# Kernel tuning notes

Hardware: AMD Instinct MI355X
Metric: run time of the kernel (lower is better)

## Reference

```python
import jax, jax.numpy as jnp
import numpy as np


def setup_inputs() -> dict:
    key = jax.random.key(0)
    k1, k2 = jax.random.split(key)
    N, H, W, F = 32, 16, 16, 256
    B, C = 64, 8
    x = jax.random.normal(k1, (N, H, W, F), dtype=jnp.float32)
    # keras 'uniform' initializer: U(-0.05, 0.05)
    T = jax.random.uniform(k2, (F, B, C), dtype=jnp.float32, minval=-0.05, maxval=0.05)
    return {"x": x, "T": T}


def reference(x, T):
    # x: [N,H,W,F], T: [F,B,C]
    M = jnp.einsum('nhwf,fbc->nhwbc', x, T)            # [N,H,W,B,C]
    # all-pairs L1 distance over C between samples i and j
    diff = jnp.abs(M[:, None] - M[None, :])            # [N,N,H,W,B,C]
    norm = jnp.sum(diff, axis=-1)                      # [N,N,H,W,B]
    o_b = jnp.sum(jnp.exp(-norm), axis=1)              # [N,H,W,B]
    return jnp.concatenate([x, o_b], axis=3)           # [N,H,W,F+B]
```

## Files before the change

kernel.cpp:

```cpp
#include <hip/hip_runtime.h>
#include <hip/hip_bf16.h>


namespace {
constexpr int kN = 32;
constexpr int kHW = 256;
constexpr int kF = 256;
constexpr int kOutRow = 320;
constexpr int kMstride = 520;
}

using frag_ab = __attribute__((ext_vector_type(8))) short;
using frag_cd = __attribute__((ext_vector_type(4))) float;

__device__ inline unsigned short f2bf(float f) {
  union { __hip_bfloat16 h; unsigned short u; } c;
  c.h = __float2bfloat16(f);
  return c.u;
}

__device__ inline void unpack8(const uint4& m, float* f) {
  f[0] = __uint_as_float(m.x << 16);  f[1] = __uint_as_float(m.x & 0xffff0000u);
  f[2] = __uint_as_float(m.y << 16);  f[3] = __uint_as_float(m.y & 0xffff0000u);
  f[4] = __uint_as_float(m.z << 16);  f[5] = __uint_as_float(m.z & 0xffff0000u);
  f[6] = __uint_as_float(m.w << 16);  f[7] = __uint_as_float(m.w & 0xffff0000u);
}

__global__ __launch_bounds__(256)
void pack_T(const float* __restrict__ T, uint4* __restrict__ Tf) {
  const int g = blockIdx.x * 256 + threadIdx.x;
  const int l = g & 63;
  const int frag = g >> 6;
  const int tt = frag >> 3, kt = frag & 7;
  const int col = tt * 16 + (l & 15);
  const int k0 = kt * 32 + (l >> 4) * 8;
  unsigned p[4];
#pragma unroll
  for (int jj = 0; jj < 4; ++jj) {
    float a = T[(size_t)(k0 + jj * 2) * 512 + col];
    float b = T[(size_t)(k0 + jj * 2 + 1) * 512 + col];
    p[jj] = (unsigned)f2bf(a) | ((unsigned)f2bf(b) << 16);
  }
  Tf[g] = make_uint4(p[0], p[1], p[2], p[3]);
}

__global__ __launch_bounds__(512, 2)
void mbd_main(const float* __restrict__ x, const uint4* __restrict__ Tf,
              float* __restrict__ out) {
  __shared__ uint4 Afrag[2 * 8 * 64];
  __shared__ __align__(16) unsigned short Mlds[kN * kMstride];
  float* obuf = (float*)Afrag;
  const int hw = blockIdx.x;
  const int tid = threadIdx.x;
  const int l = tid & 63, w = tid >> 6;

  const float4* x4 = (const float4*)x;
  float4* out4 = (float4*)out;
#pragma unroll
  for (int s = 0; s < 2; ++s) {
    const int task = tid + s * 512;
    const int n = task >> 5;
    const int k8 = task & 31;
    const size_t xb = (size_t)n * (kHW * kF / 4) + (size_t)hw * (kF / 4) + k8 * 2;
    float4 v0 = x4[xb];
    float4 v1 = x4[xb + 1];
    const size_t ob = (size_t)(n * kHW + hw) * (kOutRow / 4) + k8 * 2;
    out4[ob] = v0;
    out4[ob + 1] = v1;
    uint4 p;
    p.x = (unsigned)f2bf(v0.x) | ((unsigned)f2bf(v0.y) << 16);
    p.y = (unsigned)f2bf(v0.z) | ((unsigned)f2bf(v0.w) << 16);
    p.z = (unsigned)f2bf(v1.x) | ((unsigned)f2bf(v1.y) << 16);
    p.w = (unsigned)f2bf(v1.z) | ((unsigned)f2bf(v1.w) << 16);
    const int rt = n >> 4, kt = k8 >> 2, ln = (n & 15) | ((k8 & 3) << 4);
    Afrag[(rt * 8 + kt) * 64 + ln] = p;
  }
  __syncthreads();

  frag_cd acc[4][2] = {};
#pragma unroll
  for (int kt = 0; kt < 8; ++kt) {
    uint4 a0 = Afrag[(0 * 8 + kt) * 64 + l];
    uint4 a1 = Afrag[(1 * 8 + kt) * 64 + l];
    frag_ab af0 = __builtin_bit_cast(frag_ab, a0);
    frag_ab af1 = __builtin_bit_cast(frag_ab, a1);
#pragma unroll
    for (int q = 0; q < 4; ++q) {
      const int tT = w * 4 + q;
      uint4 b = Tf[(tT * 8 + kt) * 64 + l];
      frag_ab bf = __builtin_bit_cast(frag_ab, b);
      acc[q][0] = __builtin_amdgcn_mfma_f32_16x16x32_bf16(af0, bf, acc[q][0], 0, 0, 0);
      acc[q][1] = __builtin_amdgcn_mfma_f32_16x16x32_bf16(af1, bf, acc[q][1], 0, 0, 0);
    }
  }
  __syncthreads();

#pragma unroll
  for (int q = 0; q < 4; ++q)
#pragma unroll
    for (int rt = 0; rt < 2; ++rt)
#pragma unroll
      for (int r = 0; r < 4; ++r) {
        const int n = rt * 16 + (l >> 4) * 4 + r;
        const int t = (w * 4 + q) * 16 + (l & 15);
        Mlds[n * kMstride + t] = f2bf(acc[q][rt][r]);
      }
  __syncthreads();

  const int bA = tid >> 4;
  const int i0 = (tid & 15) * 2;
  float mi[2][2][8];
#pragma unroll
  for (int bs = 0; bs < 2; ++bs)
#pragma unroll
    for (int ii = 0; ii < 2; ++ii) {
      uint4 m = *(const uint4*)&Mlds[(i0 + ii) * kMstride + (bA + bs * 32) * 8];
      unpack8(m, mi[bs][ii]);
    }
  float ob[2][2] = {};
#pragma unroll 4
  for (int j = 0; j < kN; ++j) {
#pragma unroll
    for (int bs = 0; bs < 2; ++bs) {
      uint4 m = *(const uint4*)&Mlds[j * kMstride + (bA + bs * 32) * 8];
      float mj[8];
      unpack8(m, mj);
#pragma unroll
      for (int ii = 0; ii < 2; ++ii) {
        float nrm = 0.f;
#pragma unroll
        for (int c = 0; c < 8; ++c) nrm += fabsf(mi[bs][ii][c] - mj[c]);
        ob[bs][ii] += __expf(-nrm);
      }
    }
  }
#pragma unroll
  for (int bs = 0; bs < 2; ++bs)
#pragma unroll
    for (int ii = 0; ii < 2; ++ii)
      obuf[(i0 + ii) * 68 + bA + bs * 32] = ob[bs][ii];
  __syncthreads();
  {
    const int n = tid >> 4;
    const int b4 = tid & 15;
    float4 v = *(const float4*)&obuf[n * 68 + b4 * 4];
    out4[(size_t)(n * kHW + hw) * (kOutRow / 4) + (kF / 4) + b4] = v;
  }
}

extern "C" void kernel_launch(void* const* d_in, const int* in_sizes, int n_in,
                              void* d_out, int out_size, void* d_ws, size_t ws_size,
                              hipStream_t stream) {
  const float* x = (const float*)d_in[0];
  const float* T = (const float*)d_in[1];
  float* out = (float*)d_out;
  uint4* Tf = (uint4*)d_ws;
  (void)in_sizes; (void)n_in; (void)out_size; (void)ws_size;
  pack_T<<<dim3(64), dim3(256), 0, stream>>>(T, Tf);
  mbd_main<<<dim3(kHW), dim3(512), 0, stream>>>(x, Tf, out);
}
```

Measured before the change: 82.52 us.

## Split each pixel's work across four blocks by B-quarter to raise parallelism

```diff
diff --git a/kernel.cpp b/kernel.cpp
--- a/kernel.cpp
+++ b/kernel.cpp
@@ -7,7 +7,8 @@
 constexpr int kHW = 256;
 constexpr int kF = 256;
 constexpr int kOutRow = 320;
-constexpr int kMstride = 520;
+constexpr int kMstride = 136;
+constexpr int kOstride = 24;
 }
 
 using frag_ab = __attribute__((ext_vector_type(8))) short;
@@ -44,29 +45,41 @@
   Tf[g] = make_uint4(p[0], p[1], p[2], p[3]);
 }
 
-__global__ __launch_bounds__(512, 2)
+__global__ __launch_bounds__(256, 4)
 void mbd_main(const float* __restrict__ x, const uint4* __restrict__ Tf,
               float* __restrict__ out) {
   __shared__ uint4 Afrag[2 * 8 * 64];
   __shared__ __align__(16) unsigned short Mlds[kN * kMstride];
   float* obuf = (float*)Afrag;
-  const int hw = blockIdx.x;
+  const int hw = blockIdx.x & (kHW - 1);
+  const int qg = blockIdx.x >> 8;
   const int tid = threadIdx.x;
   const int l = tid & 63, w = tid >> 6;
+
+  uint4 bfr[2][8];
+#pragma unroll
+  for (int q = 0; q < 2; ++q)
+#pragma unroll
+    for (int kt = 0; kt < 8; ++kt) {
+      const int tT = qg * 8 + w * 2 + q;
+      bfr[q][kt] = Tf[(tT * 8 + kt) * 64 + l];
+    }
 
   const float4* x4 = (const float4*)x;
   float4* out4 = (float4*)out;
 #pragma unroll
-  for (int s = 0; s < 2; ++s) {
-    const int task = tid + s * 512;
+  for (int s = 0; s < 4; ++s) {
+    const int task = tid + s * 256;
     const int n = task >> 5;
     const int k8 = task & 31;
     const size_t xb = (size_t)n * (kHW * kF / 4) + (size_t)hw * (kF / 4) + k8 * 2;
     float4 v0 = x4[xb];
     float4 v1 = x4[xb + 1];
-    const size_t ob = (size_t)(n * kHW + hw) * (kOutRow / 4) + k8 * 2;
-    out4[ob] = v0;
-    out4[ob + 1] = v1;
+    if ((k8 >> 3) == qg) {
+      const size_t ob = (size_t)(n * kHW + hw) * (kOutRow / 4) + k8 * 2;
+      out4[ob] = v0;
+      out4[ob + 1] = v1;
+    }
     uint4 p;
     p.x = (unsigned)f2bf(v0.x) | ((unsigned)f2bf(v0.y) << 16);
     p.y = (unsigned)f2bf(v0.z) | ((unsigned)f2bf(v0.w) << 16);
@@ -77,7 +90,7 @@
   }
   __syncthreads();
 
-  frag_cd acc[4][2] = {};
+  frag_cd acc[2][2] = {};
 #pragma unroll
   for (int kt = 0; kt < 8; ++kt) {
     uint4 a0 = Afrag[(0 * 8 + kt) * 64 + l];
@@ -85,66 +98,57 @@
     frag_ab af0 = __builtin_bit_cast(frag_ab, a0);
     frag_ab af1 = __builtin_bit_cast(frag_ab, a1);
 #pragma unroll
-    for (int q = 0; q < 4; ++q) {
-      const int tT = w * 4 + q;
-      uint4 b = Tf[(tT * 8 + kt) * 64 + l];
-      frag_ab bf = __builtin_bit_cast(frag_ab, b);
+    for (int q = 0; q < 2; ++q) {
+      frag_ab bf = __builtin_bit_cast(frag_ab, bfr[q][kt]);
       acc[q][0] = __builtin_amdgcn_mfma_f32_16x16x32_bf16(af0, bf, acc[q][0], 0, 0, 0);
       acc[q][1] = __builtin_amdgcn_mfma_f32_16x16x32_bf16(af1, bf, acc[q][1], 0, 0, 0);
     }
   }
-  __syncthreads();
 
 #pragma unroll
-  for (int q = 0; q < 4; ++q)
+  for (int q = 0; q < 2; ++q)
 #pragma unroll
     for (int rt = 0; rt < 2; ++rt)
 #pragma unroll
       for (int r = 0; r < 4; ++r) {
         const int n = rt * 16 + (l >> 4) * 4 + r;
-        const int t = (w * 4 + q) * 16 + (l & 15);
+        const int t = (w * 2 + q) * 16 + (l & 15);
         Mlds[n * kMstride + t] = f2bf(acc[q][rt][r]);
       }
   __syncthreads();
 
-  const int bA = tid >> 4;
+  const int b = tid >> 4;
   const int i0 = (tid & 15) * 2;
-  float mi[2][2][8];
+  float mi[2][8];
 #pragma unroll
-  for (int bs = 0; bs < 2; ++bs)
-#pragma unroll
-    for (int ii = 0; ii < 2; ++ii) {
-      uint4 m = *(const uint4*)&Mlds[(i0 + ii) * kMstride + (bA + bs * 32) * 8];
-      unpack8(m, mi[bs][ii]);
-    }
-  float ob[2][2] = {};
+  for (int ii = 0; ii < 2; ++ii) {
+    uint4 m = *(const uint4*)&Mlds[(i0 + ii) * kMstride + b * 8];
+    unpack8(m, mi[ii]);
+  }
+  float ob0 = 0.f, ob1 = 0.f;
 #pragma unroll 4
   for (int j = 0; j < kN; ++j) {
+    uint4 m = *(const uint4*)&Mlds[j * kMstride + b * 8];
+    float mj[8];
+    unpack8(m, mj);
+    float n0 = 0.f, n1 = 0.f;
 #pragma unroll
-    for (int bs = 0; bs < 2; ++bs) {
-      uint4 m = *(const uint4*)&Mlds[j * kMstride + (bA + bs * 32) * 8];
-      float mj[8];
-      unpack8(m, mj);
-#pragma unroll
-      for (int ii = 0; ii < 2; ++ii) {
-        float nrm = 0.f;
-#pragma unroll
-        for (int c = 0; c < 8; ++c) nrm += fabsf(mi[bs][ii][c] - mj[c]);
-        ob[bs][ii] += __expf(-nrm);
-      }
+    for (int c = 0; c < 8; ++c) {
+      n0 += fabsf(mi[0][c] - mj[c]);
+      n1 += fabsf(mi[1][c] - mj[c]);
     }
+    ob0 += __expf(-n0);
+    ob1 += __expf(-n1);
   }
-#pragma unroll
-  for (int bs = 0; bs < 2; ++bs)
-#pragma unroll
-    for (int ii = 0; ii < 2; ++ii)
-      obuf[(i0 + ii) * 68 + bA + bs * 32] = ob[bs][ii];
+  obuf[i0 * kOstride + b] = ob0;
+  obuf[(i0 + 1) * kOstride + b] = ob1;
   __syncthreads();
-  {
-    const int n = tid >> 4;
-    const int b4 = tid & 15;
-    float4 v = *(const float4*)&obuf[n * 68 + b4 * 4];
-    out4[(size_t)(n * kHW + hw) * (kOutRow / 4) + (kF / 4) + b4] = v;
+
+  if (tid < 128) {
+    const int n = tid >> 2;
+    const int b4 = tid & 3;
+    float4 v = *(const float4*)&obuf[n * kOstride + b4 * 4];
+    out4[(size_t)(n * kHW + hw) * (kOutRow / 4) + (kF / 4) + qg * 4 + b4] = v;
   }
 }
 
@@ -157,5 +161,5 @@
   uint4* Tf = (uint4*)d_ws;
   (void)in_sizes; (void)n_in; (void)out_size; (void)ws_size;
   pack_T<<<dim3(64), dim3(256), 0, stream>>>(T, Tf);
-  mbd_main<<<dim3(kHW), dim3(512), 0, stream>>>(x, Tf, out);
+  mbd_main<<<dim3(4 * kHW), dim3(256), 0, stream>>>(x, Tf, out);
 }
```

Result: faster. 77.20 us (-6.4%).
